# Optimization experiments

Measured on AMD Instinct MI355X. Metric: run time of the kernel, lower is better.

## Reference

```python
import jax, jax.numpy as jnp
import numpy as np

N_NODES = 100000
N_EDGES = 1600000
D_FEAT = 64
EPS = 1e-07


def setup_inputs() -> dict:
    key = jax.random.key(0)
    k_x, k_r, k_c, k_b = jax.random.split(key, 4)
    x = jax.random.normal(k_x, (N_NODES, D_FEAT), dtype=jnp.float32)
    row = jax.random.randint(k_r, (N_EDGES,), 0, N_NODES, dtype=jnp.int64)
    col = jax.random.randint(k_c, (N_EDGES,), 0, N_NODES, dtype=jnp.int64)
    beta = jax.random.uniform(k_b, (), dtype=jnp.float32)  # nn.Parameter ~ U(0,1)
    return {"x": x, "row": row, "col": col, "beta": beta}


def segment_softmax(logits, seg_ids, num_segments):
    # numerically stable softmax over edges grouped by seg_ids
    seg_max = jax.ops.segment_max(logits, seg_ids, num_segments=num_segments)
    e = jnp.exp(logits - seg_max[seg_ids])
    seg_sum = jax.ops.segment_sum(e, seg_ids, num_segments=num_segments)
    return e / seg_sum[seg_ids]


def reference(x, row, col, beta):
    A = x[row]                       # [E, d] gather at source of softmax group
    B = x[col]                       # [E, d]
    inner = jnp.sum(A * B, axis=1)   # [E]
    denom = jnp.linalg.norm(A, axis=1) * jnp.linalg.norm(B, axis=1) + EPS
    sim = beta * (inner / denom)     # [E]
    P = segment_softmax(sim, row, N_NODES)          # softmax grouped by row
    src = A * P[:, None]                            # [E, d]
    out = jax.ops.segment_sum(src, col, num_segments=N_NODES)  # scatter-add by col
    return out
```

## Files before the change

### kernel.cpp

```cpp
#include <hip/hip_runtime.h>
#include <math.h>

#define N_NODES 100000
#define N_EDGES 1600000
#define D_FEAT 64
#define EPS 1e-7f
#define NPART 8
#define NSHARD 8
#define SPW 100032
#define COLS_PER_PART (N_NODES / NPART)
#define QSCALE 12000.0f
#define QINV (1.0f / 12000.0f)

typedef _Float16 h2 __attribute__((ext_vector_type(2)));

__device__ __forceinline__ unsigned pack2h(float a, float b) {
    h2 h;
    h.x = (_Float16)a;
    h.y = (_Float16)b;
    return __builtin_bit_cast(unsigned, h);
}

__device__ __forceinline__ float dot2acc(unsigned a, unsigned b, float c) {
#if __has_builtin(__builtin_amdgcn_fdot2)
    return __builtin_amdgcn_fdot2(__builtin_bit_cast(h2, a),
                                  __builtin_bit_cast(h2, b), c, false);
#else
    h2 ha = __builtin_bit_cast(h2, a), hb = __builtin_bit_cast(h2, b);
    return c + (float)ha.x * (float)hb.x + (float)ha.y * (float)hb.y;
#endif
}

__device__ __forceinline__ void fma2h(unsigned ab, float p, float& x, float& y) {
    h2 h = __builtin_bit_cast(h2, ab);
    x += p * (float)h.x;
    y += p * (float)h.y;
}

__device__ __forceinline__ float fastrcp(float x) {
#if __has_builtin(__builtin_amdgcn_rcpf)
    return __builtin_amdgcn_rcpf(x);
#else
    return 1.0f / x;
#endif
}

__device__ __forceinline__ unsigned enc_byte(unsigned h16) {
    unsigned s = (h16 >> 8) & 0x80u;
    unsigned a = h16 & 0x7FFFu;
    unsigned e = (a < 0x2000u) ? 0u : ((a - 0x2000u + 0x40u) >> 7);
    if (e > 0x7Eu) e = 0x7Eu;
    return s | e;
}

__device__ __forceinline__ unsigned pk4_e4m3(float a, float b, float c, float d) {
    unsigned u0 = pack2h(a, b);
    unsigned u1 = pack2h(c, d);
    return enc_byte(u0 & 0xFFFFu) | (enc_byte(u0 >> 16) << 8)
         | (enc_byte(u1 & 0xFFFFu) << 16) | (enc_byte(u1 >> 16) << 24);
}

__device__ __forceinline__ float dot4_e4m3(unsigned w, unsigned hc01, unsigned hc23, float acc) {
    unsigned p0 = ((w & 0x0080u) << 8) | ((w & 0x007Fu) << 7)
                | ((w & 0x8000u) << 16) | ((w & 0x7F00u) << 15);
    unsigned p1 = ((w >> 8) & 0x8000u) | (((w >> 16) & 0x007Fu) << 7)
                | (w & 0x80000000u) | ((w & 0x7F000000u) >> 1);
    acc = dot2acc(p0, hc01, acc);
    acc = dot2acc(p1, hc23, acc);
    return acc;
}

__device__ __forceinline__ float dot16_e4m3(uint4 A, const unsigned* hcp) {
    float d = 0.0f;
    d = dot4_e4m3(A.x, hcp[0], hcp[1], d);
    d = dot4_e4m3(A.y, hcp[2], hcp[3], d);
    d = dot4_e4m3(A.z, hcp[4], hcp[5], d);
    d = dot4_e4m3(A.w, hcp[6], hcp[7], d);
    return d;
}

__global__ void prep_kernel(const float4* __restrict__ x4, uint2* __restrict__ xh2,
                            unsigned* __restrict__ xf8, float* __restrict__ nrm,
                            const int* __restrict__ col, unsigned* __restrict__ cnt8,
                            int norm_blocks) {
    if ((int)blockIdx.x < norm_blocks) {
        int tid = blockIdx.x * blockDim.x + threadIdx.x;
        int node = tid >> 4;
        int lane = tid & 15;
        if (node >= N_NODES) return;
        float4 v = x4[(size_t)node * 16 + lane];
        uint2 h;
        h.x = pack2h(v.x, v.y);
        h.y = pack2h(v.z, v.w);
        xh2[(size_t)node * 16 + lane] = h;
        float s = v.x * v.x + v.y * v.y + v.z * v.z + v.w * v.w;
        s += __shfl_xor(s, 1);
        s += __shfl_xor(s, 2);
        s += __shfl_xor(s, 4);
        s += __shfl_xor(s, 8);
        float rn = rsqrtf(s);
        xf8[(size_t)node * 16 + lane] = pk4_e4m3(v.x * rn, v.y * rn, v.z * rn, v.w * rn);
        if (lane == 0) nrm[node] = rn;
    } else {
        int hb = blockIdx.x - norm_blocks;
        int part = hb & (NPART - 1);
        int blk = hb >> 3;
        int nblk = (gridDim.x - norm_blocks) >> 3;
        unsigned* cs = cnt8 + (size_t)(blk & (NSHARD - 1)) * SPW;
        int lo = part * COLS_PER_PART;
        int hi = lo + COLS_PER_PART;
        int stride = nblk * blockDim.x;
        const int4* col4 = (const int4*)col;
        for (int e = blk * blockDim.x + threadIdx.x; e < (N_EDGES >> 2); e += stride) {
            int4 c = col4[e];
            if (c.x >= lo && c.x < hi) atomicAdd(&cs[c.x], 1u);
            if (c.y >= lo && c.y < hi) atomicAdd(&cs[c.y], 1u);
            if (c.z >= lo && c.z < hi) atomicAdd(&cs[c.z], 1u);
            if (c.w >= lo && c.w < hi) atomicAdd(&cs[c.w], 1u);
        }
    }
}

#define SCAN_B 256
__global__ void scan1_kernel(const unsigned* __restrict__ cnt8, unsigned* __restrict__ incl,
                             unsigned* __restrict__ bsum) {
    __shared__ unsigned sh[SCAN_B];
    int i = blockIdx.x * SCAN_B + threadIdx.x;
    unsigned v = 0u;
    if (i < N_NODES) {
        #pragma unroll
        for (int k = 0; k < NSHARD; k++) v += cnt8[(size_t)k * SPW + i];
    }
    sh[threadIdx.x] = v;
    __syncthreads();
    for (int off = 1; off < SCAN_B; off <<= 1) {
        unsigned u = (threadIdx.x >= off) ? sh[threadIdx.x - off] : 0u;
        __syncthreads();
        sh[threadIdx.x] += u;
        __syncthreads();
    }
    if (i < N_NODES) incl[i] = sh[threadIdx.x];
    if (threadIdx.x == SCAN_B - 1) bsum[blockIdx.x] = sh[SCAN_B - 1];
}

__global__ void scan2_kernel(unsigned* __restrict__ bsum, int nblocks) {
    __shared__ unsigned sh[512];
    int t = threadIdx.x;
    unsigned v = (t < nblocks) ? bsum[t] : 0u;
    sh[t] = v;
    __syncthreads();
    for (int off = 1; off < 512; off <<= 1) {
        unsigned u = (t >= off) ? sh[t - off] : 0u;
        __syncthreads();
        sh[t] += u;
        __syncthreads();
    }
    if (t < nblocks) bsum[t] = sh[t] - v;
}

__global__ void scan3_kernel(unsigned* __restrict__ cnt8, const unsigned* __restrict__ incl,
                             const unsigned* __restrict__ bsum, unsigned* __restrict__ offs) {
    int i = blockIdx.x * SCAN_B + threadIdx.x;
    if (i < N_NODES) {
        unsigned c8[NSHARD];
        unsigned tot = 0u;
        #pragma unroll
        for (int k = 0; k < NSHARD; k++) { c8[k] = cnt8[(size_t)k * SPW + i]; tot += c8[k]; }
        unsigned o = bsum[blockIdx.x] + incl[i] - tot;
        offs[i] = o;
        unsigned acc = o;
        #pragma unroll
        for (int k = 0; k < NSHARD; k++) { cnt8[(size_t)k * SPW + i] = acc; acc += c8[k]; }
    } else if (i == N_NODES) {
        offs[N_NODES] = N_EDGES;
    }
}

__global__ void place_kernel(const int* __restrict__ row, const int* __restrict__ col,
                             unsigned* __restrict__ cur8, unsigned* __restrict__ pay) {
    int part = blockIdx.x & (NPART - 1);
    int blk  = blockIdx.x >> 3;
    int nblk = gridDim.x >> 3;
    unsigned* cs = cur8 + (size_t)(blk & (NSHARD - 1)) * SPW;
    int lo = part * COLS_PER_PART;
    int hi = lo + COLS_PER_PART;
    int stride = nblk * blockDim.x;
    const int4* col4 = (const int4*)col;
    for (int e4 = blk * blockDim.x + threadIdx.x; e4 < (N_EDGES >> 2); e4 += stride) {
        int4 c = col4[e4];
        int e = e4 << 2;
        if (c.x >= lo && c.x < hi) {
            unsigned pos = atomicAdd(&cs[c.x], 1u);
            pay[pos] = (unsigned)row[e] << 15;
        }
        if (c.y >= lo && c.y < hi) {
            unsigned pos = atomicAdd(&cs[c.y], 1u);
            pay[pos] = (unsigned)row[e + 1] << 15;
        }
        if (c.z >= lo && c.z < hi) {
            unsigned pos = atomicAdd(&cs[c.z], 1u);
            pay[pos] = (unsigned)row[e + 2] << 15;
        }
        if (c.w >= lo && c.w < hi) {
            unsigned pos = atomicAdd(&cs[c.w], 1u);
            pay[pos] = (unsigned)row[e + 3] << 15;
        }
    }
}

__global__ void sim_csr_kernel(const uint4* __restrict__ xf8q, const uint4* __restrict__ xh4,
                               const float* __restrict__ nrm, const unsigned* __restrict__ offs,
                               unsigned* __restrict__ pay, const float* __restrict__ beta_p,
                               float* __restrict__ segsum8) {
    int gtid = blockIdx.x * blockDim.x + threadIdx.x;
    int node = gtid >> 6;
    if (node >= N_NODES) return;
    float* seg = segsum8 + (size_t)(blockIdx.x & (NSHARD - 1)) * SPW;
    int lane = threadIdx.x & 63;
    int sub = lane >> 2;
    int fl  = lane & 3;
    uint4 hA = xh4[(size_t)node * 8 + fl * 2];
    uint4 hB = xh4[(size_t)node * 8 + fl * 2 + 1];
    float rs = nrm[node] * 256.0f;
    unsigned hcp[8];
    {
        h2 t;
        t = __builtin_bit_cast(h2, hA.x); hcp[0] = pack2h((float)t.x * rs, (float)t.y * rs);
        t = __builtin_bit_cast(h2, hA.y); hcp[1] = pack2h((float)t.x * rs, (float)t.y * rs);
        t = __builtin_bit_cast(h2, hA.z); hcp[2] = pack2h((float)t.x * rs, (float)t.y * rs);
        t = __builtin_bit_cast(h2, hA.w); hcp[3] = pack2h((float)t.x * rs, (float)t.y * rs);
        t = __builtin_bit_cast(h2, hB.x); hcp[4] = pack2h((float)t.x * rs, (float)t.y * rs);
        t = __builtin_bit_cast(h2, hB.y); hcp[5] = pack2h((float)t.x * rs, (float)t.y * rs);
        t = __builtin_bit_cast(h2, hB.z); hcp[6] = pack2h((float)t.x * rs, (float)t.y * rs);
        t = __builtin_bit_cast(h2, hB.w); hcp[7] = pack2h((float)t.x * rs, (float)t.y * rs);
    }
    float beta = beta_p[0];
    int start = (int)offs[node];
    int end = (int)offs[node + 1];
    for (int i0 = start; i0 < end; i0 += 32) {
        int idx = i0 + lane;
        if (idx > end - 1) idx = end - 1;
        unsigned pvL = pay[idx];
        unsigned pv0 = __shfl(pvL, sub);
        unsigned pv1 = __shfl(pvL, sub + 16);
        uint4 A0 = xf8q[(size_t)(pv0 >> 15) * 4 + fl];
        uint4 A1 = xf8q[(size_t)(pv1 >> 15) * 4 + fl];
        float d0 = dot16_e4m3(A0, hcp);
        float d1 = dot16_e4m3(A1, hcp);
        d0 += __shfl_xor(d0, 1);  d1 += __shfl_xor(d1, 1);
        d0 += __shfl_xor(d0, 2);  d1 += __shfl_xor(d1, 2);
        float ds = (fl & 1) ? d1 : d0;
        unsigned pvs = (fl & 1) ? pv1 : pv0;
        int ss = i0 + ((fl & 1) << 4) + sub;
        if (fl < 2 && ss < end) {
            unsigned r = pvs >> 15;
            float ex = expf(beta * ds);
            unsigned q = (unsigned)(ex * QSCALE + 0.5f);
            if (q > 32767u) q = 32767u;
            pay[ss] = pvs | q;
            atomicAdd(&seg[r], (float)q * QINV);
        }
    }
}

__global__ void xw_kernel(uint2* __restrict__ xw2, const float* __restrict__ segsum8) {
    int tid = blockIdx.x * blockDim.x + threadIdx.x;
    int node = tid >> 4;
    int il = tid & 15;
    if (node >= N_NODES) return;
    float s = (il < NSHARD) ? segsum8[(size_t)il * SPW + node] : 0.0f;
    s += __shfl_xor(s, 8);
    s += __shfl_xor(s, 4);
    s += __shfl_xor(s, 2);
    s += __shfl_xor(s, 1);
    float w = fastrcp(s);
    uint2 h = xw2[(size_t)node * 16 + il];
    h2 ha = __builtin_bit_cast(h2, h.x);
    h2 hb = __builtin_bit_cast(h2, h.y);
    uint2 o;
    o.x = pack2h((float)ha.x * w, (float)ha.y * w);
    o.y = pack2h((float)hb.x * w, (float)hb.y * w);
    xw2[(size_t)node * 16 + il] = o;
}

__global__ void gather_kernel(const uint4* __restrict__ xw4, const unsigned* __restrict__ offs,
                              const unsigned* __restrict__ pay, float4* __restrict__ out4) {
    int gtid = blockIdx.x * blockDim.x + threadIdx.x;
    int node = gtid >> 6;
    if (node >= N_NODES) return;
    int lane = threadIdx.x & 63;
    int sub = lane >> 3;
    int fl  = lane & 7;
    int start = (int)offs[node];
    int end = (int)offs[node + 1];
    float a0 = 0.f, a1 = 0.f, a2 = 0.f, a3 = 0.f;
    float a4 = 0.f, a5 = 0.f, a6 = 0.f, a7 = 0.f;
    for (int i0 = start; i0 < end; i0 += 32) {
        int idx = i0 + lane;
        if (idx > end - 1) idx = end - 1;
        unsigned pvL = pay[idx];
        unsigned pv0 = __shfl(pvL, sub);
        unsigned pv1 = __shfl(pvL, sub + 8);
        unsigned pv2 = __shfl(pvL, sub + 16);
        unsigned pv3 = __shfl(pvL, sub + 24);
        float p0 = (i0 + sub      < end) ? (float)(pv0 & 0x7FFFu) * QINV : 0.0f;
        float p1 = (i0 + sub +  8 < end) ? (float)(pv1 & 0x7FFFu) * QINV : 0.0f;
        float p2 = (i0 + sub + 16 < end) ? (float)(pv2 & 0x7FFFu) * QINV : 0.0f;
        float p3 = (i0 + sub + 24 < end) ? (float)(pv3 & 0x7FFFu) * QINV : 0.0f;
        uint4 A0 = xw4[(size_t)(pv0 >> 15) * 8 + fl];
        uint4 A1 = xw4[(size_t)(pv1 >> 15) * 8 + fl];
        uint4 A2 = xw4[(size_t)(pv2 >> 15) * 8 + fl];
        uint4 A3 = xw4[(size_t)(pv3 >> 15) * 8 + fl];
        fma2h(A0.x, p0, a0, a1); fma2h(A1.x, p1, a0, a1);
        fma2h(A2.x, p2, a0, a1); fma2h(A3.x, p3, a0, a1);
        fma2h(A0.y, p0, a2, a3); fma2h(A1.y, p1, a2, a3);
        fma2h(A2.y, p2, a2, a3); fma2h(A3.y, p3, a2, a3);
        fma2h(A0.z, p0, a4, a5); fma2h(A1.z, p1, a4, a5);
        fma2h(A2.z, p2, a4, a5); fma2h(A3.z, p3, a4, a5);
        fma2h(A0.w, p0, a6, a7); fma2h(A1.w, p1, a6, a7);
        fma2h(A2.w, p2, a6, a7); fma2h(A3.w, p3, a6, a7);
    }
    #pragma unroll
    for (int m = 8; m <= 32; m <<= 1) {
        a0 += __shfl_xor(a0, m);
        a1 += __shfl_xor(a1, m);
        a2 += __shfl_xor(a2, m);
        a3 += __shfl_xor(a3, m);
        a4 += __shfl_xor(a4, m);
        a5 += __shfl_xor(a5, m);
        a6 += __shfl_xor(a6, m);
        a7 += __shfl_xor(a7, m);
    }
    if (sub == 0) {
        out4[(size_t)node * 16 + fl * 2]     = make_float4(a0, a1, a2, a3);
        out4[(size_t)node * 16 + fl * 2 + 1] = make_float4(a4, a5, a6, a7);
    }
}

extern "C" void kernel_launch(void* const* d_in, const int* in_sizes, int n_in,
                              void* d_out, int out_size, void* d_ws, size_t ws_size,
                              hipStream_t stream) {
    const float* x      = (const float*)d_in[0];
    const int*   row    = (const int*)d_in[1];
    const int*   col    = (const int*)d_in[2];
    const float* beta_p = (const float*)d_in[3];
    const float4* x4 = (const float4*)x;
    float4* out4 = (float4*)d_out;

    const size_t E4 = (size_t)N_EDGES * 4;
    const size_t XH = (size_t)N_NODES * D_FEAT * 2;
    const size_t XF = (size_t)N_NODES * D_FEAT;
    const size_t S  = (size_t)SPW * 4;
    char* ws = (char*)d_ws;
    unsigned* pay    = (unsigned*)ws;
    uint2*    xh2    = (uint2*)(ws + E4);
    const uint4* xh4 = (const uint4*)(ws + E4);
    const uint4* xw4 = (const uint4*)(ws + E4);
    unsigned* xf8    = (unsigned*)(ws + E4 + XH);
    const uint4* xf8q = (const uint4*)(ws + E4 + XH);
    char* base2 = ws + E4 + XH + XF;
    float*    segsum8 = (float*)(base2);
    unsigned* cnt8    = (unsigned*)(base2 + 8 * S);
    float*    nrm     = (float*)(base2 + 16 * S);
    unsigned* incl    = (unsigned*)(base2 + 17 * S);
    unsigned* offs    = (unsigned*)(base2 + 18 * S);
    unsigned* bsum    = (unsigned*)(base2 + 19 * S);

    const int B = 256;
    const int nscan_blocks = (N_NODES + SCAN_B - 1) / SCAN_B;

    hipMemsetAsync(base2, 0, 16 * S, stream);

    const int norm_blocks = (N_NODES * 16 + B - 1) / B;
    const int hist_blocks = 2048;
    prep_kernel<<<norm_blocks + hist_blocks, B, 0, stream>>>(x4, xh2, xf8, nrm, col, cnt8,
                                                             norm_blocks);

    scan1_kernel<<<nscan_blocks, SCAN_B, 0, stream>>>(cnt8, incl, bsum);
    scan2_kernel<<<1, 512, 0, stream>>>(bsum, nscan_blocks);
    scan3_kernel<<<nscan_blocks + 1, SCAN_B, 0, stream>>>(cnt8, incl, bsum, offs);

    place_kernel<<<2048, B, 0, stream>>>(row, col, cnt8, pay);

    int node_wave_grid = (N_NODES * 64) / B;
    sim_csr_kernel<<<node_wave_grid, B, 0, stream>>>(xf8q, xh4, nrm, offs, pay, beta_p, segsum8);

    xw_kernel<<<norm_blocks, B, 0, stream>>>(xh2, segsum8);

    gather_kernel<<<node_wave_grid, B, 0, stream>>>(xw4, offs, pay, out4);
}
```

Before: 351.8 us.

## Split edge loops into row-range passes to localize gathered node reads

```diff
diff --git a/kernel.cpp b/kernel.cpp
--- a/kernel.cpp
+++ b/kernel.cpp
@@ -11,6 +11,8 @@
 #define COLS_PER_PART (N_NODES / NPART)
 #define QSCALE 12000.0f
 #define QINV (1.0f / 12000.0f)
+#define ROW_HALF 50000
+#define ROW_QUART 25000
 
 typedef _Float16 h2 __attribute__((ext_vector_type(2)));
 
@@ -237,28 +239,43 @@
     float beta = beta_p[0];
     int start = (int)offs[node];
     int end = (int)offs[node + 1];
-    for (int i0 = start; i0 < end; i0 += 32) {
-        int idx = i0 + lane;
-        if (idx > end - 1) idx = end - 1;
-        unsigned pvL = pay[idx];
-        unsigned pv0 = __shfl(pvL, sub);
-        unsigned pv1 = __shfl(pvL, sub + 16);
-        uint4 A0 = xf8q[(size_t)(pv0 >> 15) * 4 + fl];
-        uint4 A1 = xf8q[(size_t)(pv1 >> 15) * 4 + fl];
-        float d0 = dot16_e4m3(A0, hcp);
-        float d1 = dot16_e4m3(A1, hcp);
-        d0 += __shfl_xor(d0, 1);  d1 += __shfl_xor(d1, 1);
-        d0 += __shfl_xor(d0, 2);  d1 += __shfl_xor(d1, 2);
-        float ds = (fl & 1) ? d1 : d0;
-        unsigned pvs = (fl & 1) ? pv1 : pv0;
-        int ss = i0 + ((fl & 1) << 4) + sub;
-        if (fl < 2 && ss < end) {
-            unsigned r = pvs >> 15;
-            float ex = expf(beta * ds);
-            unsigned q = (unsigned)(ex * QSCALE + 0.5f);
-            if (q > 32767u) q = 32767u;
-            pay[ss] = pvs | q;
-            atomicAdd(&seg[r], (float)q * QINV);
+    for (int half = 0; half < 2; ++half) {
+        int rlo = half * ROW_HALF;
+        int rhi = rlo + ROW_HALF;
+        for (int i0 = start; i0 < end; i0 += 32) {
+            int idx = i0 + lane;
+            if (idx > end - 1) idx = end - 1;
+            unsigned pvL = pay[idx];
+            unsigned pv0 = __shfl(pvL, sub);
+            unsigned pv1 = __shfl(pvL, sub + 16);
+            int r0 = (int)(pv0 >> 15), r1 = (int)(pv1 >> 15);
+            bool in0 = (i0 + sub      < end) && (r0 >= rlo) && (r0 < rhi);
+            bool in1 = (i0 + sub + 16 < end) && (r1 >= rlo) && (r1 < rhi);
+            float d0 = 0.0f, d1 = 0.0f;
+            if (in0) {
+                uint4 A0 = xf8q[(size_t)r0 * 4 + fl];
+                d0 = dot16_e4m3(A0, hcp);
+                d0 += __shfl_xor(d0, 1);
+                d0 += __shfl_xor(d0, 2);
+            }
+            if (in1) {
+                uint4 A1 = xf8q[(size_t)r1 * 4 + fl];
+                d1 = dot16_e4m3(A1, hcp);
+                d1 += __shfl_xor(d1, 1);
+                d1 += __shfl_xor(d1, 2);
+            }
+            float ds = (fl & 1) ? d1 : d0;
+            unsigned pvs = (fl & 1) ? pv1 : pv0;
+            bool ins = (fl & 1) ? in1 : in0;
+            int ss = i0 + ((fl & 1) << 4) + sub;
+            if (fl < 2 && ins) {
+                unsigned r = pvs >> 15;
+                float ex = expf(beta * ds);
+                unsigned q = (unsigned)(ex * QSCALE + 0.5f);
+                if (q > 32767u) q = 32767u;
+                pay[ss] = pvs | q;
+                atomicAdd(&seg[r], (float)q * QINV);
+            }
         }
     }
 }
@@ -295,30 +312,52 @@
     int end = (int)offs[node + 1];
     float a0 = 0.f, a1 = 0.f, a2 = 0.f, a3 = 0.f;
     float a4 = 0.f, a5 = 0.f, a6 = 0.f, a7 = 0.f;
-    for (int i0 = start; i0 < end; i0 += 32) {
-        int idx = i0 + lane;
-        if (idx > end - 1) idx = end - 1;
-        unsigned pvL = pay[idx];
-        unsigned pv0 = __shfl(pvL, sub);
-        unsigned pv1 = __shfl(pvL, sub + 8);
-        unsigned pv2 = __shfl(pvL, sub + 16);
-        unsigned pv3 = __shfl(pvL, sub + 24);
-        float p0 = (i0 + sub      < end) ? (float)(pv0 & 0x7FFFu) * QINV : 0.0f;
-        float p1 = (i0 + sub +  8 < end) ? (float)(pv1 & 0x7FFFu) * QINV : 0.0f;
-        float p2 = (i0 + sub + 16 < end) ? (float)(pv2 & 0x7FFFu) * QINV : 0.0f;
-        float p3 = (i0 + sub + 24 < end) ? (float)(pv3 & 0x7FFFu) * QINV : 0.0f;
-        uint4 A0 = xw4[(size_t)(pv0 >> 15) * 8 + fl];
-        uint4 A1 = xw4[(size_t)(pv1 >> 15) * 8 + fl];
-        uint4 A2 = xw4[(size_t)(pv2 >> 15) * 8 + fl];
-        uint4 A3 = xw4[(size_t)(pv3 >> 15) * 8 + fl];
-        fma2h(A0.x, p0, a0, a1); fma2h(A1.x, p1, a0, a1);
-        fma2h(A2.x, p2, a0, a1); fma2h(A3.x, p3, a0, a1);
-        fma2h(A0.y, p0, a2, a3); fma2h(A1.y, p1, a2, a3);
-        fma2h(A2.y, p2, a2, a3); fma2h(A3.y, p3, a2, a3);
-        fma2h(A0.z, p0, a4, a5); fma2h(A1.z, p1, a4, a5);
-        fma2h(A2.z, p2, a4, a5); fma2h(A3.z, p3, a4, a5);
-        fma2h(A0.w, p0, a6, a7); fma2h(A1.w, p1, a6, a7);
-        fma2h(A2.w, p2, a6, a7); fma2h(A3.w, p3, a6, a7);
+    for (int quart = 0; quart < 4; ++quart) {
+        int rlo = quart * ROW_QUART;
+        int rhi = rlo + ROW_QUART;
+        for (int i0 = start; i0 < end; i0 += 32) {
+            int idx = i0 + lane;
+            if (idx > end - 1) idx = end - 1;
+            unsigned pvL = pay[idx];
+            unsigned pv0 = __shfl(pvL, sub);
+            unsigned pv1 = __shfl(pvL, sub + 8);
+            unsigned pv2 = __shfl(pvL, sub + 16);
+            unsigned pv3 = __shfl(pvL, sub + 24);
+            int r0 = (int)(pv0 >> 15), r1 = (int)(pv1 >> 15);
+            int r2 = (int)(pv2 >> 15), r3 = (int)(pv3 >> 15);
+            if ((i0 + sub < end) && r0 >= rlo && r0 < rhi) {
+                float p0 = (float)(pv0 & 0x7FFFu) * QINV;
+                uint4 A0 = xw4[(size_t)r0 * 8 + fl];
+                fma2h(A0.x, p0, a0, a1);
+                fma2h(A0.y, p0, a2, a3);
+                fma2h(A0.z, p0, a4, a5);
+                fma2h(A0.w, p0, a6, a7);
+            }
+            if ((i0 + sub + 8 < end) && r1 >= rlo && r1 < rhi) {
+                float p1 = (float)(pv1 & 0x7FFFu) * QINV;
+                uint4 A1 = xw4[(size_t)r1 * 8 + fl];
+                fma2h(A1.x, p1, a0, a1);
+                fma2h(A1.y, p1, a2, a3);
+                fma2h(A1.z, p1, a4, a5);
+                fma2h(A1.w, p1, a6, a7);
+            }
+            if ((i0 + sub + 16 < end) && r2 >= rlo && r2 < rhi) {
+                float p2 = (float)(pv2 & 0x7FFFu) * QINV;
+                uint4 A2 = xw4[(size_t)r2 * 8 + fl];
+                fma2h(A2.x, p2, a0, a1);
+                fma2h(A2.y, p2, a2, a3);
+                fma2h(A2.z, p2, a4, a5);
+                fma2h(A2.w, p2, a6, a7);
+            }
+            if ((i0 + sub + 24 < end) && r3 >= rlo && r3 < rhi) {
+                float p3 = (float)(pv3 & 0x7FFFu) * QINV;
+                uint4 A3 = xw4[(size_t)r3 * 8 + fl];
+                fma2h(A3.x, p3, a0, a1);
+                fma2h(A3.y, p3, a2, a3);
+                fma2h(A3.z, p3, a4, a5);
+                fma2h(A3.w, p3, a6, a7);
+            }
+        }
     }
     #pragma unroll
     for (int m = 8; m <= 32; m <<= 1) {
```

New measurement: 397.1 us. 12.9% more time.

## Shard atomics by XCC id, drop column partitioning, use integer segment sums

Applied to the files above, without the earlier changes.

```diff
diff --git a/kernel.cpp b/kernel.cpp
--- a/kernel.cpp
+++ b/kernel.cpp
@@ -5,10 +5,8 @@
 #define N_EDGES 1600000
 #define D_FEAT 64
 #define EPS 1e-7f
-#define NPART 8
 #define NSHARD 8
 #define SPW 100032
-#define COLS_PER_PART (N_NODES / NPART)
 #define QSCALE 12000.0f
 #define QINV (1.0f / 12000.0f)
 
@@ -43,6 +41,16 @@
 #else
     return 1.0f / x;
 #endif
+}
+
+#define HWREG_XCC_ID (((32 - 1) << 11) | 20)
+
+__device__ __forceinline__ unsigned xcc_shard() {
+    return (unsigned)__builtin_amdgcn_s_getreg(HWREG_XCC_ID) & (NSHARD - 1);
+}
+
+__device__ __forceinline__ void atomic_add_u32_l2(unsigned* p, unsigned v) {
+    __hip_atomic_fetch_add(p, v, __ATOMIC_RELAXED, __HIP_MEMORY_SCOPE_WORKGROUP);
 }
 
 __device__ __forceinline__ unsigned enc_byte(unsigned h16) {
@@ -103,20 +111,16 @@
         if (lane == 0) nrm[node] = rn;
     } else {
         int hb = blockIdx.x - norm_blocks;
-        int part = hb & (NPART - 1);
-        int blk = hb >> 3;
-        int nblk = (gridDim.x - norm_blocks) >> 3;
-        unsigned* cs = cnt8 + (size_t)(blk & (NSHARD - 1)) * SPW;
-        int lo = part * COLS_PER_PART;
-        int hi = lo + COLS_PER_PART;
+        int nblk = gridDim.x - norm_blocks;
+        unsigned* cs = cnt8 + (size_t)xcc_shard() * SPW;
         int stride = nblk * blockDim.x;
         const int4* col4 = (const int4*)col;
-        for (int e = blk * blockDim.x + threadIdx.x; e < (N_EDGES >> 2); e += stride) {
+        for (int e = hb * blockDim.x + threadIdx.x; e < (N_EDGES >> 2); e += stride) {
             int4 c = col4[e];
-            if (c.x >= lo && c.x < hi) atomicAdd(&cs[c.x], 1u);
-            if (c.y >= lo && c.y < hi) atomicAdd(&cs[c.y], 1u);
-            if (c.z >= lo && c.z < hi) atomicAdd(&cs[c.z], 1u);
-            if (c.w >= lo && c.w < hi) atomicAdd(&cs[c.w], 1u);
+            atomic_add_u32_l2(&cs[c.x], 1u);
+            atomic_add_u32_l2(&cs[c.y], 1u);
+            atomic_add_u32_l2(&cs[c.z], 1u);
+            atomic_add_u32_l2(&cs[c.w], 1u);
         }
     }
 }
@@ -158,64 +162,48 @@
     if (t < nblocks) bsum[t] = sh[t] - v;
 }
 
-__global__ void scan3_kernel(unsigned* __restrict__ cnt8, const unsigned* __restrict__ incl,
-                             const unsigned* __restrict__ bsum, unsigned* __restrict__ offs) {
+__global__ void scan3_kernel(const unsigned* __restrict__ cnt8, const unsigned* __restrict__ incl,
+                             const unsigned* __restrict__ bsum, unsigned* __restrict__ offs,
+                             unsigned* __restrict__ cursor) {
     int i = blockIdx.x * SCAN_B + threadIdx.x;
     if (i < N_NODES) {
-        unsigned c8[NSHARD];
         unsigned tot = 0u;
         #pragma unroll
-        for (int k = 0; k < NSHARD; k++) { c8[k] = cnt8[(size_t)k * SPW + i]; tot += c8[k]; }
+        for (int k = 0; k < NSHARD; k++) tot += cnt8[(size_t)k * SPW + i];
         unsigned o = bsum[blockIdx.x] + incl[i] - tot;
         offs[i] = o;
-        unsigned acc = o;
-        #pragma unroll
-        for (int k = 0; k < NSHARD; k++) { cnt8[(size_t)k * SPW + i] = acc; acc += c8[k]; }
+        cursor[i] = o;
     } else if (i == N_NODES) {
         offs[N_NODES] = N_EDGES;
     }
 }
 
 __global__ void place_kernel(const int* __restrict__ row, const int* __restrict__ col,
-                             unsigned* __restrict__ cur8, unsigned* __restrict__ pay) {
-    int part = blockIdx.x & (NPART - 1);
-    int blk  = blockIdx.x >> 3;
-    int nblk = gridDim.x >> 3;
-    unsigned* cs = cur8 + (size_t)(blk & (NSHARD - 1)) * SPW;
-    int lo = part * COLS_PER_PART;
-    int hi = lo + COLS_PER_PART;
-    int stride = nblk * blockDim.x;
+                             unsigned* __restrict__ cursor, unsigned* __restrict__ pay) {
+    int stride = gridDim.x * blockDim.x;
     const int4* col4 = (const int4*)col;
-    for (int e4 = blk * blockDim.x + threadIdx.x; e4 < (N_EDGES >> 2); e4 += stride) {
+    for (int e4 = blockIdx.x * blockDim.x + threadIdx.x; e4 < (N_EDGES >> 2); e4 += stride) {
         int4 c = col4[e4];
         int e = e4 << 2;
-        if (c.x >= lo && c.x < hi) {
-            unsigned pos = atomicAdd(&cs[c.x], 1u);
-            pay[pos] = (unsigned)row[e] << 15;
-        }
-        if (c.y >= lo && c.y < hi) {
-            unsigned pos = atomicAdd(&cs[c.y], 1u);
-            pay[pos] = (unsigned)row[e + 1] << 15;
-        }
-        if (c.z >= lo && c.z < hi) {
-            unsigned pos = atomicAdd(&cs[c.z], 1u);
-            pay[pos] = (unsigned)row[e + 2] << 15;
-        }
-        if (c.w >= lo && c.w < hi) {
-            unsigned pos = atomicAdd(&cs[c.w], 1u);
-            pay[pos] = (unsigned)row[e + 3] << 15;
-        }
+        unsigned p0 = atomicAdd(&cursor[c.x], 1u);
+        pay[p0] = (unsigned)row[e] << 15;
+        unsigned p1 = atomicAdd(&cursor[c.y], 1u);
+        pay[p1] = (unsigned)row[e + 1] << 15;
+        unsigned p2 = atomicAdd(&cursor[c.z], 1u);
+        pay[p2] = (unsigned)row[e + 2] << 15;
+        unsigned p3 = atomicAdd(&cursor[c.w], 1u);
+        pay[p3] = (unsigned)row[e + 3] << 15;
     }
 }
 
 __global__ void sim_csr_kernel(const uint4* __restrict__ xf8q, const uint4* __restrict__ xh4,
                                const float* __restrict__ nrm, const unsigned* __restrict__ offs,
                                unsigned* __restrict__ pay, const float* __restrict__ beta_p,
-                               float* __restrict__ segsum8) {
+                               unsigned* __restrict__ segsum8) {
     int gtid = blockIdx.x * blockDim.x + threadIdx.x;
     int node = gtid >> 6;
     if (node >= N_NODES) return;
-    float* seg = segsum8 + (size_t)(blockIdx.x & (NSHARD - 1)) * SPW;
+    unsigned* seg = segsum8 + (size_t)xcc_shard() * SPW;
     int lane = threadIdx.x & 63;
     int sub = lane >> 2;
     int fl  = lane & 3;
@@ -258,22 +246,22 @@
             unsigned q = (unsigned)(ex * QSCALE + 0.5f);
             if (q > 32767u) q = 32767u;
             pay[ss] = pvs | q;
-            atomicAdd(&seg[r], (float)q * QINV);
+            atomic_add_u32_l2(&seg[r], q);
         }
     }
 }
 
-__global__ void xw_kernel(uint2* __restrict__ xw2, const float* __restrict__ segsum8) {
+__global__ void xw_kernel(uint2* __restrict__ xw2, const unsigned* __restrict__ segsum8) {
     int tid = blockIdx.x * blockDim.x + threadIdx.x;
     int node = tid >> 4;
     int il = tid & 15;
     if (node >= N_NODES) return;
-    float s = (il < NSHARD) ? segsum8[(size_t)il * SPW + node] : 0.0f;
+    unsigned s = (il < NSHARD) ? segsum8[(size_t)il * SPW + node] : 0u;
     s += __shfl_xor(s, 8);
     s += __shfl_xor(s, 4);
     s += __shfl_xor(s, 2);
     s += __shfl_xor(s, 1);
-    float w = fastrcp(s);
+    float w = fastrcp((float)s * QINV);
     uint2 h = xw2[(size_t)node * 16 + il];
     h2 ha = __builtin_bit_cast(h2, h.x);
     h2 hb = __builtin_bit_cast(h2, h.y);
@@ -359,12 +347,13 @@
     unsigned* xf8    = (unsigned*)(ws + E4 + XH);
     const uint4* xf8q = (const uint4*)(ws + E4 + XH);
     char* base2 = ws + E4 + XH + XF;
-    float*    segsum8 = (float*)(base2);
+    unsigned* segsum8 = (unsigned*)(base2);
     unsigned* cnt8    = (unsigned*)(base2 + 8 * S);
     float*    nrm     = (float*)(base2 + 16 * S);
     unsigned* incl    = (unsigned*)(base2 + 17 * S);
     unsigned* offs    = (unsigned*)(base2 + 18 * S);
-    unsigned* bsum    = (unsigned*)(base2 + 19 * S);
+    unsigned* cursor  = (unsigned*)(base2 + 19 * S);
+    unsigned* bsum    = (unsigned*)(base2 + 20 * S);
 
     const int B = 256;
     const int nscan_blocks = (N_NODES + SCAN_B - 1) / SCAN_B;
@@ -378,9 +367,9 @@
 
     scan1_kernel<<<nscan_blocks, SCAN_B, 0, stream>>>(cnt8, incl, bsum);
     scan2_kernel<<<1, 512, 0, stream>>>(bsum, nscan_blocks);
-    scan3_kernel<<<nscan_blocks + 1, SCAN_B, 0, stream>>>(cnt8, incl, bsum, offs);
-
-    place_kernel<<<2048, B, 0, stream>>>(row, col, cnt8, pay);
+    scan3_kernel<<<nscan_blocks + 1, SCAN_B, 0, stream>>>(cnt8, incl, bsum, offs, cursor);
+
+    place_kernel<<<2048, B, 0, stream>>>(row, col, cursor, pay);
 
     int node_wave_grid = (N_NODES * 64) / B;
     sim_csr_kernel<<<node_wave_grid, B, 0, stream>>>(xf8q, xh4, nrm, offs, pay, beta_p, segsum8);
```

New measurement: 380.3 us. +8.1%, slower.
